# Kernel tuning notes

Measured on AMD Instinct MI355X. Metric: run time of the kernel, lower is better.

Reference implementation:

```python
import jax, jax.numpy as jnp
import numpy as np

B, E, N = 4, 100000, 10000          # batch copies, edges, nodes
NR, H, D, OUT, L = 6, 256, 256, 128, 3  # num_radial, hidden, out_emb, out, num_layers


def setup_inputs() -> dict:
    key = jax.random.key(0)
    ks = jax.random.split(key, 7)
    x = jax.random.normal(ks[0], (B, E, H), dtype=jnp.float32)
    rbf = jax.random.normal(ks[1], (E, NR), dtype=jnp.float32)
    i = jax.random.randint(ks[2], (E,), 0, N, dtype=jnp.int32)
    # Learned params (stored transposed vs torch Linear: [in, out])
    W_rbf = jax.random.normal(ks[3], (NR, H), dtype=jnp.float32) / np.float32(np.sqrt(NR))
    W_up = jax.random.normal(ks[4], (H, D), dtype=jnp.float32) / np.float32(np.sqrt(H))
    Ws = jax.random.normal(ks[5], (L, D, D), dtype=jnp.float32) / np.float32(np.sqrt(D))
    bs = jnp.zeros((L, D), dtype=jnp.float32)
    W_out = jax.random.normal(ks[6], (D, OUT), dtype=jnp.float32) / np.float32(np.sqrt(D))
    return {"x": x, "rbf": rbf, "i": i, "W_rbf": W_rbf, "W_up": W_up,
            "Ws": Ws, "bs": bs, "W_out": W_out, "num_nodes": N}


def reference(x, rbf, i, W_rbf, W_up, Ws, bs, W_out, num_nodes):
    # x: [B,E,H], rbf: [E,NR], i: [E]
    g = (rbf @ W_rbf)[None, :, :] * x            # lin_rbf(rbf) * x -> [B,E,H]
    # scatter-sum over edges into nodes (dim=1)
    agg = jax.vmap(lambda xb: jax.ops.segment_sum(xb, i, num_segments=num_nodes))(g)  # [B,N,H]
    h = agg @ W_up                               # lin_up (no bias) -> [B,N,D]
    for l in range(Ws.shape[0]):                 # small fixed layer stack
        h = jax.nn.silu(h @ Ws[l] + bs[l])
    return h @ W_out                             # lin (no bias) -> [B,N,OUT]
```

## Files before the change

### kernel.cpp

```cpp
#include <hip/hip_runtime.h>
#include <hip/hip_bf16.h>

#define B_  4
#define E_  100000
#define N_  10000
#define NR_ 6
#define H_  256
#define D_  256
#define OUT_ 128

typedef __attribute__((ext_vector_type(4))) float f32x4;
typedef __attribute__((ext_vector_type(8))) short bf16x8;

__device__ __forceinline__ ushort f2bf(float f) {
  unsigned u = __builtin_bit_cast(unsigned, f);
  u += 0x7fffu + ((u >> 16) & 1u);
  return (ushort)(u >> 16);
}

__global__ __launch_bounds__(256) void hist_kernel(const int* __restrict__ idx,
                                                   int* __restrict__ counts) {
  int e = blockIdx.x * 256 + threadIdx.x;
  if (e < E_) atomicAdd(&counts[idx[e]], 1);
}

__global__ __launch_bounds__(1024) void scan_kernel(
    const int* __restrict__ counts, int* __restrict__ starts,
    int* __restrict__ cursor) {
  __shared__ int sums[1024];
  const int t = threadIdx.x;
  const int base = t * 10;
  int loc[10];
  int s = 0;
#pragma unroll
  for (int j = 0; j < 10; ++j) {
    int v = (base + j < N_) ? counts[base + j] : 0;
    loc[j] = v;
    s += v;
  }
  sums[t] = s;
  __syncthreads();
  for (int off = 1; off < 1024; off <<= 1) {
    int v = (t >= off) ? sums[t - off] : 0;
    __syncthreads();
    sums[t] += v;
    __syncthreads();
  }
  int run = sums[t] - s;
#pragma unroll
  for (int j = 0; j < 10; ++j) {
    if (base + j < N_) {
      starts[base + j] = run;
      cursor[base + j] = run;
      run += loc[j];
    }
  }
}

__global__ __launch_bounds__(256) void fill_kernel(const int* __restrict__ idx,
                                                   int* __restrict__ cursor,
                                                   int* __restrict__ buckets) {
  int e = blockIdx.x * 256 + threadIdx.x;
  if (e < E_) {
    int pos = atomicAdd(&cursor[idx[e]], 1);
    buckets[pos] = e;
  }
}

__global__ __launch_bounds__(256) void gather_kernel(
    const float* __restrict__ x, const float* __restrict__ rbf,
    const float* __restrict__ W_rbf, const int* __restrict__ starts,
    const int* __restrict__ counts, const int* __restrict__ buckets,
    ushort* __restrict__ agg) {
  __shared__ int elds[256];
  const int node = blockIdx.x;
  const int tid = threadIdx.x;
  const int b = tid >> 6;
  const int t = tid & 63;
  const int h0 = t * 4;

  f32x4 wrv[NR_];
#pragma unroll
  for (int r = 0; r < NR_; ++r)
    wrv[r] = *reinterpret_cast<const f32x4*>(&W_rbf[r * H_ + h0]);

  f32x4 acc = {0.f, 0.f, 0.f, 0.f};
  const int s = starts[node];
  const int d = counts[node];

  for (int c0 = 0; c0 < d; c0 += 256) {
    const int nc = min(256, d - c0);
    __syncthreads();
    if (tid < nc) elds[tid] = buckets[s + c0 + tid];
    __syncthreads();
#pragma unroll 4
    for (int j = 0; j < nc; ++j) {
      const int e = elds[j];
      f32x4 rp = {0.f, 0.f, 0.f, 0.f};
#pragma unroll
      for (int r = 0; r < NR_; ++r) rp += rbf[e * NR_ + r] * wrv[r];
      const f32x4 xv = *reinterpret_cast<const f32x4*>(
          &x[((size_t)b * E_ + e) * H_ + h0]);
      acc += xv * rp;
    }
  }

  ushort4 o;
  o.x = f2bf(acc.x); o.y = f2bf(acc.y); o.z = f2bf(acc.z); o.w = f2bf(acc.w);
  *reinterpret_cast<ushort4*>(&agg[((size_t)b * N_ + node) * H_ + h0]) = o;
}

__global__ __launch_bounds__(256) void convert_weights(
    const float* __restrict__ W_up, const float* __restrict__ Ws,
    const float* __restrict__ W_out, ushort* __restrict__ Wp) {
  const int g = blockIdx.x * 256 + threadIdx.x;
  int l, goff, Ncols;
  if (g < 32768) { l = g >> 13; goff = g & 8191; Ncols = 256; }
  else           { l = 4;       goff = g - 32768; Ncols = 128; }
  const float* src = (l == 0) ? W_up : (l < 4 ? Ws + (l - 1) * 65536 : W_out);
  const int lane = goff & 63;
  const int ks   = (goff >> 6) & 7;
  const int nb   = goff >> 9;
  const int col  = nb * 16 + (lane & 15);
  const int k0   = ks * 32 + (lane >> 4) * 8;
  ushort tmp[8];
#pragma unroll
  for (int j = 0; j < 8; ++j)
    tmp[j] = f2bf(src[(size_t)(k0 + j) * Ncols + col]);
  *reinterpret_cast<uint4*>(&Wp[(size_t)g * 8]) =
      *reinterpret_cast<const uint4*>(tmp);
}

__global__ __launch_bounds__(512) void chain_kernel(
    const ushort* __restrict__ agg, const ushort* __restrict__ Wp,
    const float* __restrict__ bs, float* __restrict__ out) {
  __shared__ ushort act[64 * 256];
  char* actb = reinterpret_cast<char*>(act);
  const int row0 = blockIdx.x * 64;
  const int tid = threadIdx.x;
  const int wave = tid >> 6;
  const int lane = tid & 63;
  const int lr = lane & 15;
  const int lq = lane >> 4;
  const int wr = wave >> 2;
  const int wc = wave & 3;

#pragma unroll
  for (int t = 0; t < 4; ++t) {
    const int idx = tid + t * 512;
    const int row = idx >> 5;
    const int s = idx & 31;
    const uint4 v = *reinterpret_cast<const uint4*>(
        &agg[(size_t)(row0 + row) * 256 + s * 8]);
    const int byte = (row * 512 + s * 16) ^ ((row & 7) << 4);
    *reinterpret_cast<uint4*>(actb + byte) = v;
  }
  __syncthreads();

  for (int l = 0; l < 4; ++l) {
    const ushort* W = Wp + l * 65536;
    f32x4 acc[2][4] = {};
#pragma unroll
    for (int ks = 0; ks < 8; ++ks) {
      bf16x8 af[2], bfr[4];
#pragma unroll
      for (int m = 0; m < 2; ++m) {
        const int row = wr * 32 + m * 16 + lr;
        const int byte = (row * 512 + ks * 64 + lq * 16) ^ ((row & 7) << 4);
        af[m] = *reinterpret_cast<const bf16x8*>(actb + byte);
      }
#pragma unroll
      for (int n = 0; n < 4; ++n) {
        const int nb = wc * 4 + n;
        bfr[n] = *reinterpret_cast<const bf16x8*>(
            &W[(size_t)(((nb * 8 + ks) * 64) + lane) * 8]);
      }
#pragma unroll
      for (int m = 0; m < 2; ++m)
#pragma unroll
        for (int n = 0; n < 4; ++n)
          acc[m][n] = __builtin_amdgcn_mfma_f32_16x16x32_bf16(af[m], bfr[n],
                                                              acc[m][n], 0, 0, 0);
    }
    __syncthreads();

    const bool ba = (l > 0);
#pragma unroll
    for (int n = 0; n < 4; ++n) {
      const int col = wc * 64 + n * 16 + lr;
      const float bv = ba ? bs[(l - 1) * 256 + col] : 0.f;
#pragma unroll
      for (int m = 0; m < 2; ++m) {
#pragma unroll
        for (int r = 0; r < 4; ++r) {
          float v = acc[m][n][r];
          if (ba) {
            v += bv;
            v = v / (1.0f + __expf(-v));
          }
          const int row = wr * 32 + m * 16 + lq * 4 + r;
          const int byte = (row * 512 + col * 2) ^ ((row & 7) << 4);
          *reinterpret_cast<ushort*>(actb + byte) = f2bf(v);
        }
      }
    }
    __syncthreads();
  }

  {
    const ushort* W = Wp + 4 * 65536;
    f32x4 acc[2][2] = {};
#pragma unroll
    for (int ks = 0; ks < 8; ++ks) {
      bf16x8 af[2], bfr[2];
#pragma unroll
      for (int m = 0; m < 2; ++m) {
        const int row = wr * 32 + m * 16 + lr;
        const int byte = (row * 512 + ks * 64 + lq * 16) ^ ((row & 7) << 4);
        af[m] = *reinterpret_cast<const bf16x8*>(actb + byte);
      }
#pragma unroll
      for (int n = 0; n < 2; ++n) {
        const int nb = wc * 2 + n;
        bfr[n] = *reinterpret_cast<const bf16x8*>(
            &W[(size_t)(((nb * 8 + ks) * 64) + lane) * 8]);
      }
#pragma unroll
      for (int m = 0; m < 2; ++m)
#pragma unroll
        for (int n = 0; n < 2; ++n)
          acc[m][n] = __builtin_amdgcn_mfma_f32_16x16x32_bf16(af[m], bfr[n],
                                                              acc[m][n], 0, 0, 0);
    }
#pragma unroll
    for (int m = 0; m < 2; ++m)
#pragma unroll
      for (int n = 0; n < 2; ++n)
#pragma unroll
        for (int r = 0; r < 4; ++r) {
          const int row = row0 + wr * 32 + m * 16 + lq * 4 + r;
          const int col = wc * 32 + n * 16 + lr;
          out[(size_t)row * OUT_ + col] = acc[m][n][r];
        }
  }
}

extern "C" void kernel_launch(void* const* d_in, const int* in_sizes, int n_in,
                              void* d_out, int out_size, void* d_ws,
                              size_t ws_size, hipStream_t stream) {
  const float* x     = (const float*)d_in[0];
  const float* rbf   = (const float*)d_in[1];
  const int*   idx   = (const int*)d_in[2];
  const float* W_rbf = (const float*)d_in[3];
  const float* W_up  = (const float*)d_in[4];
  const float* Ws    = (const float*)d_in[5];
  const float* bs    = (const float*)d_in[6];
  const float* W_out = (const float*)d_in[7];
  float* out = (float*)d_out;

  char* ws = (char*)d_ws;
  const size_t agg_bytes = (size_t)B_ * N_ * H_ * sizeof(ushort);
  ushort* agg = (ushort*)(ws);
  ushort* Wp  = (ushort*)(ws + agg_bytes);
  char* ibase = ws + agg_bytes + 294912 * sizeof(ushort);
  int* counts  = (int*)(ibase);
  int* starts  = (int*)(ibase + 40000);
  int* cursor  = (int*)(ibase + 80000);
  int* buckets = (int*)(ibase + 120000);

  hipMemsetAsync(counts, 0, N_ * sizeof(int), stream);
  hist_kernel<<<(E_ + 255) / 256, 256, 0, stream>>>(idx, counts);
  scan_kernel<<<1, 1024, 0, stream>>>(counts, starts, cursor);
  fill_kernel<<<(E_ + 255) / 256, 256, 0, stream>>>(idx, cursor, buckets);

  convert_weights<<<36864 / 256, 256, 0, stream>>>(W_up, Ws, W_out, Wp);

  gather_kernel<<<N_, 256, 0, stream>>>(x, rbf, W_rbf, starts, counts, buckets,
                                        agg);

  chain_kernel<<<625, 512, 0, stream>>>(agg, Wp, bs, out);
}
```

Measured before the change: 195.8 us.

## Gather one node per wave across all batches; fuse histogram with weight conversion

The gather kernel now assigns one node per wavefront, four nodes per block, and each lane accumulates all four batch copies. The rbf projection and the bucket index are therefore computed once per edge instead of once per batch. This drops the shared-memory staging and its block barriers, and cuts the block count by four. The histogram and weight-conversion kernels are merged into one launch split by block index, saving a launch; the cost is more registers per thread and per-wave load imbalance on high-degree nodes.

```diff
diff --git a/kernel.cpp b/kernel.cpp
--- a/kernel.cpp
+++ b/kernel.cpp
@@ -18,102 +18,16 @@
   return (ushort)(u >> 16);
 }
 
-__global__ __launch_bounds__(256) void hist_kernel(const int* __restrict__ idx,
-                                                   int* __restrict__ counts) {
-  int e = blockIdx.x * 256 + threadIdx.x;
-  if (e < E_) atomicAdd(&counts[idx[e]], 1);
-}
-
-__global__ __launch_bounds__(1024) void scan_kernel(
-    const int* __restrict__ counts, int* __restrict__ starts,
-    int* __restrict__ cursor) {
-  __shared__ int sums[1024];
-  const int t = threadIdx.x;
-  const int base = t * 10;
-  int loc[10];
-  int s = 0;
-#pragma unroll
-  for (int j = 0; j < 10; ++j) {
-    int v = (base + j < N_) ? counts[base + j] : 0;
-    loc[j] = v;
-    s += v;
-  }
-  sums[t] = s;
-  __syncthreads();
-  for (int off = 1; off < 1024; off <<= 1) {
-    int v = (t >= off) ? sums[t - off] : 0;
-    __syncthreads();
-    sums[t] += v;
-    __syncthreads();
-  }
-  int run = sums[t] - s;
-#pragma unroll
-  for (int j = 0; j < 10; ++j) {
-    if (base + j < N_) {
-      starts[base + j] = run;
-      cursor[base + j] = run;
-      run += loc[j];
-    }
-  }
-}
-
-__global__ __launch_bounds__(256) void fill_kernel(const int* __restrict__ idx,
-                                                   int* __restrict__ cursor,
-                                                   int* __restrict__ buckets) {
-  int e = blockIdx.x * 256 + threadIdx.x;
-  if (e < E_) {
-    int pos = atomicAdd(&cursor[idx[e]], 1);
-    buckets[pos] = e;
-  }
-}
-
-__global__ __launch_bounds__(256) void gather_kernel(
-    const float* __restrict__ x, const float* __restrict__ rbf,
-    const float* __restrict__ W_rbf, const int* __restrict__ starts,
-    const int* __restrict__ counts, const int* __restrict__ buckets,
-    ushort* __restrict__ agg) {
-  __shared__ int elds[256];
-  const int node = blockIdx.x;
-  const int tid = threadIdx.x;
-  const int b = tid >> 6;
-  const int t = tid & 63;
-  const int h0 = t * 4;
-
-  f32x4 wrv[NR_];
-#pragma unroll
-  for (int r = 0; r < NR_; ++r)
-    wrv[r] = *reinterpret_cast<const f32x4*>(&W_rbf[r * H_ + h0]);
-
-  f32x4 acc = {0.f, 0.f, 0.f, 0.f};
-  const int s = starts[node];
-  const int d = counts[node];
-
-  for (int c0 = 0; c0 < d; c0 += 256) {
-    const int nc = min(256, d - c0);
-    __syncthreads();
-    if (tid < nc) elds[tid] = buckets[s + c0 + tid];
-    __syncthreads();
-#pragma unroll 4
-    for (int j = 0; j < nc; ++j) {
-      const int e = elds[j];
-      f32x4 rp = {0.f, 0.f, 0.f, 0.f};
-#pragma unroll
-      for (int r = 0; r < NR_; ++r) rp += rbf[e * NR_ + r] * wrv[r];
-      const f32x4 xv = *reinterpret_cast<const f32x4*>(
-          &x[((size_t)b * E_ + e) * H_ + h0]);
-      acc += xv * rp;
-    }
-  }
-
-  ushort4 o;
-  o.x = f2bf(acc.x); o.y = f2bf(acc.y); o.z = f2bf(acc.z); o.w = f2bf(acc.w);
-  *reinterpret_cast<ushort4*>(&agg[((size_t)b * N_ + node) * H_ + h0]) = o;
-}
-
-__global__ __launch_bounds__(256) void convert_weights(
+__global__ __launch_bounds__(256) void hist_convert_kernel(
+    const int* __restrict__ idx, int* __restrict__ counts,
     const float* __restrict__ W_up, const float* __restrict__ Ws,
     const float* __restrict__ W_out, ushort* __restrict__ Wp) {
-  const int g = blockIdx.x * 256 + threadIdx.x;
+  if (blockIdx.x < 391) {
+    const int e = blockIdx.x * 256 + threadIdx.x;
+    if (e < E_) atomicAdd(&counts[idx[e]], 1);
+    return;
+  }
+  const int g = (blockIdx.x - 391) * 256 + threadIdx.x;
   int l, goff, Ncols;
   if (g < 32768) { l = g >> 13; goff = g & 8191; Ncols = 256; }
   else           { l = 4;       goff = g - 32768; Ncols = 128; }
@@ -129,6 +43,91 @@
     tmp[j] = f2bf(src[(size_t)(k0 + j) * Ncols + col]);
   *reinterpret_cast<uint4*>(&Wp[(size_t)g * 8]) =
       *reinterpret_cast<const uint4*>(tmp);
+}
+
+__global__ __launch_bounds__(1024) void scan_kernel(
+    const int* __restrict__ counts, int* __restrict__ starts,
+    int* __restrict__ cursor) {
+  __shared__ int sums[1024];
+  const int t = threadIdx.x;
+  const int base = t * 10;
+  int loc[10];
+  int s = 0;
+#pragma unroll
+  for (int j = 0; j < 10; ++j) {
+    int v = (base + j < N_) ? counts[base + j] : 0;
+    loc[j] = v;
+    s += v;
+  }
+  sums[t] = s;
+  __syncthreads();
+  for (int off = 1; off < 1024; off <<= 1) {
+    int v = (t >= off) ? sums[t - off] : 0;
+    __syncthreads();
+    sums[t] += v;
+    __syncthreads();
+  }
+  int run = sums[t] - s;
+#pragma unroll
+  for (int j = 0; j < 10; ++j) {
+    if (base + j < N_) {
+      starts[base + j] = run;
+      cursor[base + j] = run;
+      run += loc[j];
+    }
+  }
+}
+
+__global__ __launch_bounds__(256) void fill_kernel(const int* __restrict__ idx,
+                                                   int* __restrict__ cursor,
+                                                   int* __restrict__ buckets) {
+  int e = blockIdx.x * 256 + threadIdx.x;
+  if (e < E_) {
+    int pos = atomicAdd(&cursor[idx[e]], 1);
+    buckets[pos] = e;
+  }
+}
+
+__global__ __launch_bounds__(256) void gather_kernel(
+    const float* __restrict__ x, const float* __restrict__ rbf,
+    const float* __restrict__ W_rbf, const int* __restrict__ starts,
+    const int* __restrict__ counts, const int* __restrict__ buckets,
+    ushort* __restrict__ agg) {
+  const int tid = threadIdx.x;
+  const int node = blockIdx.x * 4 + (tid >> 6);
+  const int lane = tid & 63;
+  const int h0 = lane * 4;
+
+  f32x4 wrv[NR_];
+#pragma unroll
+  for (int r = 0; r < NR_; ++r)
+    wrv[r] = *reinterpret_cast<const f32x4*>(&W_rbf[r * H_ + h0]);
+
+  f32x4 acc[B_] = {};
+  const int s = starts[node];
+  const int d = counts[node];
+
+#pragma unroll 2
+  for (int j = 0; j < d; ++j) {
+    const int e = buckets[s + j];
+    f32x4 rp = {0.f, 0.f, 0.f, 0.f};
+#pragma unroll
+    for (int r = 0; r < NR_; ++r) rp += rbf[e * NR_ + r] * wrv[r];
+#pragma unroll
+    for (int b = 0; b < B_; ++b) {
+      const f32x4 xv = *reinterpret_cast<const f32x4*>(
+          &x[((size_t)b * E_ + e) * H_ + h0]);
+      acc[b] += xv * rp;
+    }
+  }
+
+#pragma unroll
+  for (int b = 0; b < B_; ++b) {
+    ushort4 o;
+    o.x = f2bf(acc[b].x); o.y = f2bf(acc[b].y);
+    o.z = f2bf(acc[b].z); o.w = f2bf(acc[b].w);
+    *reinterpret_cast<ushort4*>(&agg[((size_t)b * N_ + node) * H_ + h0]) = o;
+  }
 }
 
 __global__ __launch_bounds__(512) void chain_kernel(
@@ -269,14 +268,13 @@
   int* buckets = (int*)(ibase + 120000);
 
   hipMemsetAsync(counts, 0, N_ * sizeof(int), stream);
-  hist_kernel<<<(E_ + 255) / 256, 256, 0, stream>>>(idx, counts);
+  hist_convert_kernel<<<391 + 144, 256, 0, stream>>>(idx, counts, W_up, Ws,
+                                                     W_out, Wp);
   scan_kernel<<<1, 1024, 0, stream>>>(counts, starts, cursor);
   fill_kernel<<<(E_ + 255) / 256, 256, 0, stream>>>(idx, cursor, buckets);
 
-  convert_weights<<<36864 / 256, 256, 0, stream>>>(W_up, Ws, W_out, Wp);
-
-  gather_kernel<<<N_, 256, 0, stream>>>(x, rbf, W_rbf, starts, counts, buckets,
-                                        agg);
+  gather_kernel<<<N_ / 4, 256, 0, stream>>>(x, rbf, W_rbf, starts, counts,
+                                            buckets, agg);
 
   chain_kernel<<<625, 512, 0, stream>>>(agg, Wp, bs, out);
 }
```

Result: no change. 199.6 us (+1.9%).
